# Performance work log

Hardware: AMD Instinct MI355X
Metric: run time of the kernel (lower is better)

## Reference

```python
import jax, jax.numpy as jnp
import numpy as np

EMBED_DIM = 1024
NUM_HEADS = 16
HEAD_DIM = EMBED_DIM // NUM_HEADS
SCALING = HEAD_DIM ** (-0.5)
SEQ = 2048
BSZ = 2


def setup_inputs() -> dict:
    key = jax.random.key(0)
    ks = jax.random.split(key, 11)
    d = {
        "query": jax.random.normal(ks[0], (SEQ, BSZ, EMBED_DIM), dtype=jnp.float32),
        "key": jax.random.normal(ks[1], (SEQ, BSZ, EMBED_DIM), dtype=jnp.float32),
        "value": jax.random.normal(ks[2], (SEQ, BSZ, EMBED_DIM), dtype=jnp.float32),
        "bias_q": jax.random.normal(ks[3], (SEQ, EMBED_DIM), dtype=jnp.float32),
        "bias_k": jax.random.normal(ks[4], (SEQ, EMBED_DIM), dtype=jnp.float32),
        "bias_v": jax.random.normal(ks[5], (SEQ, EMBED_DIM), dtype=jnp.float32),
        # Linear weights (out, in); xavier-ish scale
        "Wq": jax.random.normal(ks[6], (EMBED_DIM, EMBED_DIM), dtype=jnp.float32) * (1.0 / np.sqrt(2 * EMBED_DIM)),
        "Wk": jax.random.normal(ks[7], (EMBED_DIM, EMBED_DIM), dtype=jnp.float32) * (1.0 / np.sqrt(2 * EMBED_DIM)),
        "Wv": jax.random.normal(ks[8], (EMBED_DIM, EMBED_DIM), dtype=jnp.float32) * (1.0 / np.sqrt(2 * EMBED_DIM)),
        "Wo": jax.random.normal(ks[9], (EMBED_DIM, EMBED_DIM), dtype=jnp.float32) * (1.0 / np.sqrt(EMBED_DIM)),
        "bo": jnp.zeros((EMBED_DIM,), dtype=jnp.float32),
    }
    return d


def reference(query, key, value, bias_q, bias_k, bias_v, Wq, Wk, Wv, Wo, bo):
    tgt_len, bsz, embed_dim = query.shape
    # self_attention=True: q, k, v all projected from `query`
    q = (query @ Wq.T + bias_q[:, None, :]) * SCALING   # [T,B,E]
    k = query @ Wk.T + bias_k[:, None, :]                # [T,B,E]
    v = query @ Wv.T + bias_v[:, None, :]                # [T,B,E]

    def split_heads(x):  # [T,B,E] -> [B*H, T, Dh]
        return x.reshape(tgt_len, bsz * NUM_HEADS, HEAD_DIM).transpose(1, 0, 2)

    q, k, v = split_heads(q), split_heads(k), split_heads(v)
    attn_weights = jnp.einsum('btd,bsd->bts', q, k)      # [B*H, T, S]
    attn_weights = jax.nn.softmax(attn_weights, axis=-1)
    attn = jnp.einsum('bts,bsd->btd', attn_weights, v)   # [B*H, T, Dh]
    attn = attn.transpose(1, 0, 2).reshape(tgt_len, bsz, embed_dim)
    attn = attn @ Wo.T + bo
    return (attn, attn_weights)
```

## Files before the change

### kernel.cpp

```cpp
#include <hip/hip_runtime.h>
#include <hip/hip_fp16.h>
#include <cmath>

#define SEQLEN 2048
#define BATCH 2
#define EMB 1024
#define NHEAD 16
#define DHEAD 64
#define NBH 32
#define NROWS 4096

typedef _Float16 f16;
typedef __attribute__((ext_vector_type(4))) _Float16 f16x4;
typedef __attribute__((ext_vector_type(8))) _Float16 f16x8;
typedef __attribute__((ext_vector_type(4))) float f32x4;

__device__ __forceinline__ void gload_lds16(const f16* g, f16* l) {
    __builtin_amdgcn_global_load_lds(
        (const __attribute__((address_space(1))) void*)g,
        (__attribute__((address_space(3))) void*)l, 16, 0, 0);
}

#define QN4 1048576
#define WN4 262144
__global__ __launch_bounds__(256) void cvt_all_kernel(
    const float* __restrict__ query, const float* __restrict__ w0,
    const float* __restrict__ w1, const float* __restrict__ w2,
    const float* __restrict__ w3,
    f16* __restrict__ xh, f16* __restrict__ o0, f16* __restrict__ o1,
    f16* __restrict__ o2, f16* __restrict__ o3)
{
    const int total = QN4 + 4 * WN4;
    for (int i = blockIdx.x * 256 + threadIdx.x; i < total; i += 2048 * 256) {
        const float* src; f16* dst; int off;
        if (i < QN4) { src = query; dst = xh; off = i; }
        else {
            int j = i - QN4;
            int sel = j >> 18;
            off = j & (WN4 - 1);
            switch (sel) {
                case 0: src = w0; dst = o0; break;
                case 1: src = w1; dst = o1; break;
                case 2: src = w2; dst = o2; break;
                default: src = w3; dst = o3; break;
            }
        }
        float4 v = reinterpret_cast<const float4*>(src)[off];
        f16x4 o = {(_Float16)v.x, (_Float16)v.y, (_Float16)v.z, (_Float16)v.w};
        reinterpret_cast<f16x4*>(dst)[off] = o;
    }
}

#define PBK 32

__global__ __launch_bounds__(256, 3) void proj_kernel(
    const f16* __restrict__ xh,
    const f16* __restrict__ Wqh, const f16* __restrict__ Wkh, const f16* __restrict__ Wvh,
    const float* __restrict__ bq, const float* __restrict__ bk, const float* __restrict__ bv,
    f16* __restrict__ qh, f16* __restrict__ kh, f16* __restrict__ vT)
{
    __shared__ __align__(16) f16 smem[16384];

    const int c0f = blockIdx.y * 128;
    const int mode = c0f >> 10;
    const int c0 = c0f & 1023;
    const f16* __restrict__ W = (mode == 0) ? Wqh : (mode == 1 ? Wkh : Wvh);
    const float* __restrict__ bias = (mode == 0) ? bq : (mode == 1 ? bk : bv);
    const int r0 = blockIdx.x * 128;
    const int w = threadIdx.x >> 6;
    const int lane = threadIdx.x & 63;
    const int lr = lane & 15, lg = lane >> 4;
    const int wr = w >> 1, wc = w & 1;

    const int cA0 = w * 64 + lane;
    const int cA1 = 256 + w * 64 + lane;
    const f16* gA0 = xh + (size_t)(r0 + (cA0 >> 2)) * EMB + (cA0 & 3) * 8;
    const f16* gA1 = xh + (size_t)(r0 + (cA1 >> 2)) * EMB + (cA1 & 3) * 8;
    const f16* gB0 = W + (size_t)(c0 + (cA0 >> 2)) * EMB + (cA0 & 3) * 8;
    const f16* gB1 = W + (size_t)(c0 + (cA1 >> 2)) * EMB + (cA1 & 3) * 8;
    const int lds0 = (w * 64) * 8;
    const int lds1 = (256 + w * 64) * 8;

    f32x4 acc[4][4] = {};
    int cur = 0;

    gload_lds16(gA0, smem + lds0);
    gload_lds16(gA1, smem + lds1);
    gload_lds16(gB0, smem + 8192 + lds0);
    gload_lds16(gB1, smem + 8192 + lds1);
    __syncthreads();

    for (int kt = 0; kt < EMB / PBK; ++kt) {
        if (kt + 1 < EMB / PBK) {
            const int ko = (kt + 1) * PBK;
            const int nxt = (cur ^ 1) * 4096;
            gload_lds16(gA0 + ko, smem + nxt + lds0);
            gload_lds16(gA1 + ko, smem + nxt + lds1);
            gload_lds16(gB0 + ko, smem + 8192 + nxt + lds0);
            gload_lds16(gB1 + ko, smem + 8192 + nxt + lds1);
        }
        const f16* Ac = smem + cur * 4096;
        const f16* Bc = smem + 8192 + cur * 4096;
        f16x8 a[4], b[4];
#pragma unroll
        for (int m = 0; m < 4; ++m)
            a[m] = *reinterpret_cast<const f16x8*>(
                &Ac[(wr * 64 + m * 16 + lr) * PBK + lg * 8]);
#pragma unroll
        for (int n = 0; n < 4; ++n)
            b[n] = *reinterpret_cast<const f16x8*>(
                &Bc[(wc * 64 + n * 16 + lr) * PBK + lg * 8]);
#pragma unroll
        for (int m = 0; m < 4; ++m)
#pragma unroll
            for (int n = 0; n < 4; ++n)
                acc[m][n] = __builtin_amdgcn_mfma_f32_16x16x32_f16(b[n], a[m], acc[m][n], 0, 0, 0);
        __syncthreads();
        cur ^= 1;
    }

    if (mode != 2) {
        f16* __restrict__ dst = (mode == 0) ? qh : kh;
        const float sc = (mode == 0) ? 0.125f : 1.0f;
#pragma unroll
        for (int m = 0; m < 4; ++m) {
            const int row = r0 + wr * 64 + m * 16 + lr;
            const int t = row >> 1, bb = row & 1;
#pragma unroll
            for (int n = 0; n < 4; ++n) {
                const int col0 = c0 + wc * 64 + n * 16 + lg * 4;
                float4 b4 = *reinterpret_cast<const float4*>(&bias[(size_t)t * EMB + col0]);
                f16x4 pk = {(_Float16)((acc[m][n][0] + b4.x) * sc),
                            (_Float16)((acc[m][n][1] + b4.y) * sc),
                            (_Float16)((acc[m][n][2] + b4.z) * sc),
                            (_Float16)((acc[m][n][3] + b4.w) * sc)};
                const int h = col0 >> 6, d0 = col0 & 63;
                const int bhi = bb * NHEAD + h;
                *reinterpret_cast<f16x4*>(
                    &dst[((size_t)bhi * SEQLEN + t) * DHEAD + d0]) = pk;
            }
        }
    } else {
        f16* T = smem;
#pragma unroll
        for (int p = 0; p < 2; ++p) {
            if (wr == p) {
#pragma unroll
                for (int m = 0; m < 4; ++m) {
                    const int row = r0 + p * 64 + m * 16 + lr;
                    const int t = row >> 1;
#pragma unroll
                    for (int n = 0; n < 4; ++n) {
                        const int ci0 = wc * 64 + n * 16 + lg * 4;
                        float4 b4 = *reinterpret_cast<const float4*>(
                            &bias[(size_t)t * EMB + c0 + ci0]);
                        f16x4 pk = {(_Float16)(acc[m][n][0] + b4.x),
                                    (_Float16)(acc[m][n][1] + b4.y),
                                    (_Float16)(acc[m][n][2] + b4.z),
                                    (_Float16)(acc[m][n][3] + b4.w)};
                        *reinterpret_cast<f16x4*>(&T[(m * 16 + lr) * 132 + ci0]) = pk;
                    }
                }
            }
            __syncthreads();
            {
                const int dd = threadIdx.x & 63;
                const int hh = (threadIdx.x >> 6) & 1;
                const int bb2 = threadIdx.x >> 7;
                const int bhi2 = bb2 * NHEAD + ((c0 + hh * 64) >> 6);
                const int tbase = (r0 + p * 64) >> 1;
                f16* __restrict__ vrow =
                    vT + ((size_t)bhi2 * 64 + (tbase >> 5)) * (DHEAD * 32) + dd * 32;
#pragma unroll
                for (int j8 = 0; j8 < 4; ++j8) {
                    f16x8 pk8;
#pragma unroll
                    for (int jj = 0; jj < 8; ++jj)
                        pk8[jj] = T[(bb2 + 2 * (j8 * 8 + jj)) * 132 + hh * 64 + dd];
                    *reinterpret_cast<f16x8*>(&vrow[j8 * 8]) = pk8;
                }
            }
            __syncthreads();
        }
    }
}

#define QBLK 32
#define SCHUNK 128
#define TP 136
#define RP 2080

__global__ __launch_bounds__(1024, 1) void attn_kernel(
    const f16* __restrict__ qh, const f16* __restrict__ kh, const f16* __restrict__ vT,
    float* __restrict__ Pout, f16* __restrict__ ctx)
{
    __shared__ __align__(16) f16 tbuf[16][QBLK * TP];
    __shared__ float lsum[QBLK][16];
    __shared__ float inv_l[QBLK];
    float* red = (float*)&tbuf[0][0];

    const int id = blockIdx.x;
    const int idx = id >> 3;
    const int bh = ((id & 7) << 2) + (idx >> 6);
    const int t0 = (idx & 63) * QBLK;

    const int w = threadIdx.x >> 6;
    const int lane = threadIdx.x & 63;
    const int lr = lane & 15, lg = lane >> 4;
    const int sbase = w * SCHUNK;

    const f16* __restrict__ qb = qh + (size_t)bh * SEQLEN * DHEAD;
    const f16* __restrict__ kb = kh + (size_t)bh * SEQLEN * DHEAD;
    const f16* __restrict__ vb = vT + (size_t)bh * DHEAD * SEQLEN;

    f16x8 qf[2][2];
#pragma unroll
    for (int tt = 0; tt < 2; ++tt)
#pragma unroll
        for (int kc = 0; kc < 2; ++kc)
            qf[tt][kc] = *reinterpret_cast<const f16x8*>(
                qb + (size_t)(t0 + tt * 16 + lr) * DHEAD + kc * 32 + lg * 8);

    f16x4 ev[2][8];
    float rowsum[2] = {0.f, 0.f};
#pragma unroll
    for (int st = 0; st < 8; ++st) {
        const f16* krow = kb + (size_t)(sbase + st * 16 + lr) * DHEAD;
        f16x8 kf0 = *reinterpret_cast<const f16x8*>(krow + lg * 8);
        f16x8 kf1 = *reinterpret_cast<const f16x8*>(krow + 32 + lg * 8);
#pragma unroll
        for (int tt = 0; tt < 2; ++tt) {
            f32x4 sa = {};
            sa = __builtin_amdgcn_mfma_f32_16x16x32_f16(kf0, qf[tt][0], sa, 0, 0, 0);
            sa = __builtin_amdgcn_mfma_f32_16x16x32_f16(kf1, qf[tt][1], sa, 0, 0, 0);
            float ps = 0.f;
#pragma unroll
            for (int e = 0; e < 4; ++e) {
                float Ev = __expf(sa[e]) * 0.0625f;
                ev[tt][st][e] = (_Float16)Ev;
                ps += Ev;
            }
            rowsum[tt] += ps;
        }
    }

#pragma unroll
    for (int tt = 0; tt < 2; ++tt) {
        float v = rowsum[tt];
        v += __shfl_xor(v, 16);
        v += __shfl_xor(v, 32);
        if (lg == 0) lsum[tt * 16 + lr][w] = v;
    }

    f16* mybuf = &tbuf[w][0];
#pragma unroll
    for (int tt = 0; tt < 2; ++tt)
#pragma unroll
        for (int st = 0; st < 8; ++st)
            *reinterpret_cast<f16x4*>(
                &mybuf[(tt * 16 + lr) * TP + st * 16 + lg * 4]) = ev[tt][st];

    __syncthreads();
    if (threadIdx.x < QBLK) {
        float s = 0.f;
#pragma unroll
        for (int i = 0; i < 16; ++i) s += lsum[threadIdx.x][i];
        inv_l[threadIdx.x] = 1.0f / s;
    }
    __syncthreads();

    float* __restrict__ Pt =
        Pout + (size_t)bh * SEQLEN * SEQLEN + (size_t)t0 * SEQLEN;
#pragma unroll
    for (int j = 0; j < 2; ++j) {
        const int t = w * 2 + j;
        const float inv = inv_l[t];
#pragma unroll
        for (int cc = 0; cc < 8; ++cc) {
            const int chunk = cc * 2 + (lane >> 5);
            const int col = (lane & 31) * 4;
            f16x4 e4 = *reinterpret_cast<const f16x4*>(
                &tbuf[chunk][t * TP + col]);
            f32x4 o = {(float)e4[0] * inv, (float)e4[1] * inv,
                       (float)e4[2] * inv, (float)e4[3] * inv};
            __builtin_nontemporal_store(o,
                reinterpret_cast<f32x4*>(&Pt[(size_t)t * SEQLEN + cc * 256 + lane * 4]));
        }
    }

    f32x4 accO[2][4] = {};
#pragma unroll
    for (int c = 0; c < 4; ++c) {
        f16x8 pa0 = *reinterpret_cast<const f16x8*>(&mybuf[lr * TP + c * 32 + lg * 8]);
        f16x8 pa1 = *reinterpret_cast<const f16x8*>(&mybuf[(16 + lr) * TP + c * 32 + lg * 8]);
        const f16* vchunk = vb + (size_t)(w * 4 + c) * (DHEAD * 32);
#pragma unroll
        for (int dt = 0; dt < 4; ++dt) {
            f16x8 vf = *reinterpret_cast<const f16x8*>(
                vchunk + (dt * 16 + lr) * 32 + lg * 8);
            accO[0][dt] = __builtin_amdgcn_mfma_f32_16x16x32_f16(pa0, vf, accO[0][dt], 0, 0, 0);
            accO[1][dt] = __builtin_amdgcn_mfma_f32_16x16x32_f16(pa1, vf, accO[1][dt], 0, 0, 0);
        }
    }
    __syncthreads();

#pragma unroll
    for (int tt = 0; tt < 2; ++tt)
#pragma unroll
        for (int dt = 0; dt < 4; ++dt)
#pragma unroll
            for (int e = 0; e < 4; ++e)
                red[(size_t)w * RP + (tt * 16 + lg * 4 + e) * 65 + dt * 16 + lr] =
                    accO[tt][dt][e];
    __syncthreads();

    const int b = bh >> 4, h = bh & 15;
    for (int o = threadIdx.x; o < QBLK * DHEAD; o += 1024) {
        const int t = o >> 6, d = o & 63;
        float s = 0.f;
#pragma unroll
        for (int i = 0; i < 16; ++i) s += red[(size_t)i * RP + t * 65 + d];
        s *= inv_l[t];
        ctx[(size_t)((t0 + t) * BATCH + b) * EMB + h * DHEAD + d] = (f16)s;
    }
}

__global__ __launch_bounds__(256, 4) void oproj_kernel(
    const f16* __restrict__ ctx, const f16* __restrict__ Woh,
    const float* __restrict__ bo, float* __restrict__ out)
{
    __shared__ __align__(16) f16 smem[12288];
    const int r0 = blockIdx.x * 64;
    const int c0 = blockIdx.y * 128;
    const int w = threadIdx.x >> 6;
    const int lane = threadIdx.x & 63;
    const int lr = lane & 15, lg = lane >> 4;
    const int wr = w >> 1, wc = w & 1;

    const int cA = threadIdx.x;
    const f16* gA = ctx + (size_t)(r0 + (cA >> 2)) * EMB + (cA & 3) * 8;
    const f16* gB0 = Woh + (size_t)(c0 + (cA >> 2)) * EMB + (cA & 3) * 8;
    const f16* gB1 = Woh + (size_t)(c0 + 64 + (cA >> 2)) * EMB + (cA & 3) * 8;
    const int ldsA = (w * 64) * 8;
    const int ldsB0 = (w * 64) * 8;
    const int ldsB1 = (256 + w * 64) * 8;

    f32x4 acc[2][4] = {};
    int cur = 0;

    gload_lds16(gA, smem + ldsA);
    gload_lds16(gB0, smem + 4096 + ldsB0);
    gload_lds16(gB1, smem + 4096 + ldsB1);
    __syncthreads();

    for (int kt = 0; kt < EMB / PBK; ++kt) {
        if (kt + 1 < EMB / PBK) {
            const int ko = (kt + 1) * PBK;
            const int nxtA = (cur ^ 1) * 2048;
            const int nxtB = 4096 + (cur ^ 1) * 4096;
            gload_lds16(gA + ko, smem + nxtA + ldsA);
            gload_lds16(gB0 + ko, smem + nxtB + ldsB0);
            gload_lds16(gB1 + ko, smem + nxtB + ldsB1);
        }
        const f16* Ac = smem + cur * 2048;
        const f16* Bc = smem + 4096 + cur * 4096;
        f16x8 a[2], b[4];
#pragma unroll
        for (int m = 0; m < 2; ++m)
            a[m] = *reinterpret_cast<const f16x8*>(
                &Ac[(wr * 32 + m * 16 + lr) * PBK + lg * 8]);
#pragma unroll
        for (int n = 0; n < 4; ++n)
            b[n] = *reinterpret_cast<const f16x8*>(
                &Bc[(wc * 64 + n * 16 + lr) * PBK + lg * 8]);
#pragma unroll
        for (int m = 0; m < 2; ++m)
#pragma unroll
            for (int n = 0; n < 4; ++n)
                acc[m][n] = __builtin_amdgcn_mfma_f32_16x16x32_f16(b[n], a[m], acc[m][n], 0, 0, 0);
        __syncthreads();
        cur ^= 1;
    }

#pragma unroll
    for (int m = 0; m < 2; ++m) {
        const int row = r0 + wr * 32 + m * 16 + lr;
#pragma unroll
        for (int n = 0; n < 4; ++n) {
            const int col0 = c0 + wc * 64 + n * 16 + lg * 4;
            float4 b4 = *reinterpret_cast<const float4*>(&bo[col0]);
            f32x4 o = {acc[m][n][0] + b4.x, acc[m][n][1] + b4.y,
                       acc[m][n][2] + b4.z, acc[m][n][3] + b4.w};
            __builtin_nontemporal_store(o,
                reinterpret_cast<f32x4*>(&out[(size_t)row * EMB + col0]));
        }
    }
}

extern "C" void kernel_launch(void* const* d_in, const int* in_sizes, int n_in,
                              void* d_out, int out_size, void* d_ws, size_t ws_size,
                              hipStream_t stream) {
    const float* query = (const float*)d_in[0];
    const float* bq = (const float*)d_in[3];
    const float* bk = (const float*)d_in[4];
    const float* bv = (const float*)d_in[5];
    const float* Wq = (const float*)d_in[6];
    const float* Wk = (const float*)d_in[7];
    const float* Wv = (const float*)d_in[8];
    const float* Wo = (const float*)d_in[9];
    const float* bo = (const float*)d_in[10];

    char* ws = (char*)d_ws;
    f16* xh  = (f16*)(ws);
    f16* Wqh = (f16*)(ws + ( 8u << 20));
    f16* Wkh = (f16*)(ws + (10u << 20));
    f16* Wvh = (f16*)(ws + (12u << 20));
    f16* Woh = (f16*)(ws + (14u << 20));
    f16* qhp = (f16*)(ws + (16u << 20));
    f16* khp = (f16*)(ws + (24u << 20));
    f16* vTp = (f16*)(ws + (32u << 20));
    f16* ctx = (f16*)(ws + (40u << 20));

    float* outA = (float*)d_out;
    float* outP = (float*)d_out + (size_t)SEQLEN * BATCH * EMB;

    cvt_all_kernel<<<2048, 256, 0, stream>>>(query, Wq, Wk, Wv, Wo,
                                             xh, Wqh, Wkh, Wvh, Woh);

    proj_kernel<<<dim3(NROWS / 128, 3072 / 128), 256, 0, stream>>>(
        xh, Wqh, Wkh, Wvh, bq, bk, bv, qhp, khp, vTp);

    attn_kernel<<<SEQLEN / QBLK * NBH, 1024, 0, stream>>>(qhp, khp, vTp, outP, ctx);

    oproj_kernel<<<dim3(NROWS / 64, EMB / 128), 256, 0, stream>>>(ctx, Woh, bo, outA);
}
```

Measured before the change: 228.1 us.

## Double query block per attention CTA and overlap P stores with PV MFMAs

Each attention block now processes 64 query rows instead of 32, halving the grid and the number of times each K/V chunk is read per head. Because LDS only holds eight wave chunks at once, the waves are split into two halves. One half writes the normalized probability matrix to global memory while the other half runs the P·V MFMAs, then the roles swap after the second half of the exp values is staged. The cross-wave reduction of the output is done in two passes to fit the LDS budget. In exchange, each wave keeps twice as many registers live (ev and accO), and the extra barriers may hurt occupancy and scheduling.

```diff
diff --git a/kernel.cpp b/kernel.cpp
--- a/kernel.cpp
+++ b/kernel.cpp
@@ -185,24 +185,25 @@
     }
 }
 
-#define QBLK 32
+#define QBLK 64
 #define SCHUNK 128
 #define TP 136
+#define CHSZ (QBLK * TP)
 #define RP 2080
 
 __global__ __launch_bounds__(1024, 1) void attn_kernel(
     const f16* __restrict__ qh, const f16* __restrict__ kh, const f16* __restrict__ vT,
     float* __restrict__ Pout, f16* __restrict__ ctx)
 {
-    __shared__ __align__(16) f16 tbuf[16][QBLK * TP];
+    __shared__ __align__(16) f16 tbuf[8 * CHSZ];
     __shared__ float lsum[QBLK][16];
     __shared__ float inv_l[QBLK];
-    float* red = (float*)&tbuf[0][0];
+    float* red = (float*)&tbuf[0];
 
     const int id = blockIdx.x;
     const int idx = id >> 3;
-    const int bh = ((id & 7) << 2) + (idx >> 6);
-    const int t0 = (idx & 63) * QBLK;
+    const int bh = ((id & 7) << 2) + (idx >> 5);
+    const int t0 = (idx & 31) * QBLK;
 
     const int w = threadIdx.x >> 6;
     const int lane = threadIdx.x & 63;
@@ -213,23 +214,23 @@
     const f16* __restrict__ kb = kh + (size_t)bh * SEQLEN * DHEAD;
     const f16* __restrict__ vb = vT + (size_t)bh * DHEAD * SEQLEN;
 
-    f16x8 qf[2][2];
-#pragma unroll
-    for (int tt = 0; tt < 2; ++tt)
+    f16x8 qf[4][2];
+#pragma unroll
+    for (int tt = 0; tt < 4; ++tt)
 #pragma unroll
         for (int kc = 0; kc < 2; ++kc)
             qf[tt][kc] = *reinterpret_cast<const f16x8*>(
                 qb + (size_t)(t0 + tt * 16 + lr) * DHEAD + kc * 32 + lg * 8);
 
-    f16x4 ev[2][8];
-    float rowsum[2] = {0.f, 0.f};
+    f16x4 ev[4][8];
+    float rowsum[4] = {0.f, 0.f, 0.f, 0.f};
 #pragma unroll
     for (int st = 0; st < 8; ++st) {
         const f16* krow = kb + (size_t)(sbase + st * 16 + lr) * DHEAD;
         f16x8 kf0 = *reinterpret_cast<const f16x8*>(krow + lg * 8);
         f16x8 kf1 = *reinterpret_cast<const f16x8*>(krow + 32 + lg * 8);
 #pragma unroll
-        for (int tt = 0; tt < 2; ++tt) {
+        for (int tt = 0; tt < 4; ++tt) {
             f32x4 sa = {};
             sa = __builtin_amdgcn_mfma_f32_16x16x32_f16(kf0, qf[tt][0], sa, 0, 0, 0);
             sa = __builtin_amdgcn_mfma_f32_16x16x32_f16(kf1, qf[tt][1], sa, 0, 0, 0);
@@ -245,21 +246,22 @@
     }
 
 #pragma unroll
-    for (int tt = 0; tt < 2; ++tt) {
+    for (int tt = 0; tt < 4; ++tt) {
         float v = rowsum[tt];
         v += __shfl_xor(v, 16);
         v += __shfl_xor(v, 32);
         if (lg == 0) lsum[tt * 16 + lr][w] = v;
     }
 
-    f16* mybuf = &tbuf[w][0];
-#pragma unroll
-    for (int tt = 0; tt < 2; ++tt)
-#pragma unroll
-        for (int st = 0; st < 8; ++st)
-            *reinterpret_cast<f16x4*>(
-                &mybuf[(tt * 16 + lr) * TP + st * 16 + lg * 4]) = ev[tt][st];
-
+    if (w < 8) {
+        f16* mybuf = &tbuf[w * CHSZ];
+#pragma unroll
+        for (int tt = 0; tt < 4; ++tt)
+#pragma unroll
+            for (int st = 0; st < 8; ++st)
+                *reinterpret_cast<f16x4*>(
+                    &mybuf[(tt * 16 + lr) * TP + st * 16 + lg * 4]) = ev[tt][st];
+    }
     __syncthreads();
     if (threadIdx.x < QBLK) {
         float s = 0.f;
@@ -271,57 +273,126 @@
 
     float* __restrict__ Pt =
         Pout + (size_t)bh * SEQLEN * SEQLEN + (size_t)t0 * SEQLEN;
-#pragma unroll
-    for (int j = 0; j < 2; ++j) {
-        const int t = w * 2 + j;
-        const float inv = inv_l[t];
-#pragma unroll
-        for (int cc = 0; cc < 8; ++cc) {
-            const int chunk = cc * 2 + (lane >> 5);
-            const int col = (lane & 31) * 4;
-            f16x4 e4 = *reinterpret_cast<const f16x4*>(
-                &tbuf[chunk][t * TP + col]);
-            f32x4 o = {(float)e4[0] * inv, (float)e4[1] * inv,
-                       (float)e4[2] * inv, (float)e4[3] * inv};
-            __builtin_nontemporal_store(o,
-                reinterpret_cast<f32x4*>(&Pt[(size_t)t * SEQLEN + cc * 256 + lane * 4]));
-        }
-    }
-
-    f32x4 accO[2][4] = {};
-#pragma unroll
-    for (int c = 0; c < 4; ++c) {
-        f16x8 pa0 = *reinterpret_cast<const f16x8*>(&mybuf[lr * TP + c * 32 + lg * 8]);
-        f16x8 pa1 = *reinterpret_cast<const f16x8*>(&mybuf[(16 + lr) * TP + c * 32 + lg * 8]);
-        const f16* vchunk = vb + (size_t)(w * 4 + c) * (DHEAD * 32);
-#pragma unroll
-        for (int dt = 0; dt < 4; ++dt) {
-            f16x8 vf = *reinterpret_cast<const f16x8*>(
-                vchunk + (dt * 16 + lr) * 32 + lg * 8);
-            accO[0][dt] = __builtin_amdgcn_mfma_f32_16x16x32_f16(pa0, vf, accO[0][dt], 0, 0, 0);
-            accO[1][dt] = __builtin_amdgcn_mfma_f32_16x16x32_f16(pa1, vf, accO[1][dt], 0, 0, 0);
-        }
-    }
-    __syncthreads();
-
-#pragma unroll
-    for (int tt = 0; tt < 2; ++tt)
-#pragma unroll
-        for (int dt = 0; dt < 4; ++dt)
-#pragma unroll
-            for (int e = 0; e < 4; ++e)
-                red[(size_t)w * RP + (tt * 16 + lg * 4 + e) * 65 + dt * 16 + lr] =
-                    accO[tt][dt][e];
+    f32x4 accO[4][4] = {};
+
+    if (w >= 8) {
+        const int r0w = (w - 8) * 8;
+#pragma unroll
+        for (int r = 0; r < 8; ++r) {
+            const int t = r0w + r;
+            const float inv = inv_l[t];
+#pragma unroll
+            for (int i = 0; i < 4; ++i) {
+                const int chunk = i * 2 + (lane >> 5);
+                const int col = (lane & 31) * 4;
+                f16x4 e4 = *reinterpret_cast<const f16x4*>(
+                    &tbuf[chunk * CHSZ + t * TP + col]);
+                f32x4 o = {(float)e4[0] * inv, (float)e4[1] * inv,
+                           (float)e4[2] * inv, (float)e4[3] * inv};
+                __builtin_nontemporal_store(o,
+                    reinterpret_cast<f32x4*>(&Pt[(size_t)t * SEQLEN + i * 256 + lane * 4]));
+            }
+        }
+    } else {
+        const f16* mybuf = &tbuf[w * CHSZ];
+#pragma unroll
+        for (int c = 0; c < 4; ++c) {
+            const f16* vchunk = vb + (size_t)(w * 4 + c) * (DHEAD * 32);
+            f16x8 vf[4];
+#pragma unroll
+            for (int dt = 0; dt < 4; ++dt)
+                vf[dt] = *reinterpret_cast<const f16x8*>(
+                    vchunk + (dt * 16 + lr) * 32 + lg * 8);
+#pragma unroll
+            for (int tt = 0; tt < 4; ++tt) {
+                f16x8 pa = *reinterpret_cast<const f16x8*>(
+                    &mybuf[(tt * 16 + lr) * TP + c * 32 + lg * 8]);
+#pragma unroll
+                for (int dt = 0; dt < 4; ++dt)
+                    accO[tt][dt] = __builtin_amdgcn_mfma_f32_16x16x32_f16(
+                        pa, vf[dt], accO[tt][dt], 0, 0, 0);
+            }
+        }
+    }
+    __syncthreads();
+
+    if (w >= 8) {
+        f16* mybuf = &tbuf[(w - 8) * CHSZ];
+#pragma unroll
+        for (int tt = 0; tt < 4; ++tt)
+#pragma unroll
+            for (int st = 0; st < 8; ++st)
+                *reinterpret_cast<f16x4*>(
+                    &mybuf[(tt * 16 + lr) * TP + st * 16 + lg * 4]) = ev[tt][st];
+    }
+    __syncthreads();
+
+    if (w < 8) {
+        const int r0w = w * 8;
+#pragma unroll
+        for (int r = 0; r < 8; ++r) {
+            const int t = r0w + r;
+            const float inv = inv_l[t];
+#pragma unroll
+            for (int i = 0; i < 4; ++i) {
+                const int chunk = i * 2 + (lane >> 5);
+                const int col = (lane & 31) * 4;
+                f16x4 e4 = *reinterpret_cast<const f16x4*>(
+                    &tbuf[chunk * CHSZ + t * TP + col]);
+                f32x4 o = {(float)e4[0] * inv, (float)e4[1] * inv,
+                           (float)e4[2] * inv, (float)e4[3] * inv};
+                __builtin_nontemporal_store(o,
+                    reinterpret_cast<f32x4*>(
+                        &Pt[(size_t)t * SEQLEN + 1024 + i * 256 + lane * 4]));
+            }
+        }
+    } else {
+        const f16* mybuf = &tbuf[(w - 8) * CHSZ];
+#pragma unroll
+        for (int c = 0; c < 4; ++c) {
+            const f16* vchunk = vb + (size_t)(w * 4 + c) * (DHEAD * 32);
+            f16x8 vf[4];
+#pragma unroll
+            for (int dt = 0; dt < 4; ++dt)
+                vf[dt] = *reinterpret_cast<const f16x8*>(
+                    vchunk + (dt * 16 + lr) * 32 + lg * 8);
+#pragma unroll
+            for (int tt = 0; tt < 4; ++tt) {
+                f16x8 pa = *reinterpret_cast<const f16x8*>(
+                    &mybuf[(tt * 16 + lr) * TP + c * 32 + lg * 8]);
+#pragma unroll
+                for (int dt = 0; dt < 4; ++dt)
+                    accO[tt][dt] = __builtin_amdgcn_mfma_f32_16x16x32_f16(
+                        pa, vf[dt], accO[tt][dt], 0, 0, 0);
+            }
+        }
+    }
     __syncthreads();
 
     const int b = bh >> 4, h = bh & 15;
-    for (int o = threadIdx.x; o < QBLK * DHEAD; o += 1024) {
-        const int t = o >> 6, d = o & 63;
-        float s = 0.f;
-#pragma unroll
-        for (int i = 0; i < 16; ++i) s += red[(size_t)i * RP + t * 65 + d];
-        s *= inv_l[t];
-        ctx[(size_t)((t0 + t) * BATCH + b) * EMB + h * DHEAD + d] = (f16)s;
+#pragma unroll
+    for (int half = 0; half < 2; ++half) {
+#pragma unroll
+        for (int tl = 0; tl < 2; ++tl) {
+            const int tt = half * 2 + tl;
+#pragma unroll
+            for (int dt = 0; dt < 4; ++dt)
+#pragma unroll
+                for (int e = 0; e < 4; ++e)
+                    red[(size_t)w * RP + (tl * 16 + lg * 4 + e) * 65 + dt * 16 + lr] =
+                        accO[tt][dt][e];
+        }
+        __syncthreads();
+        for (int o = threadIdx.x; o < 32 * DHEAD; o += 1024) {
+            const int t = o >> 6, d = o & 63;
+            float s = 0.f;
+#pragma unroll
+            for (int i = 0; i < 16; ++i) s += red[(size_t)i * RP + t * 65 + d];
+            const int tg = half * 32 + t;
+            s *= inv_l[tg];
+            ctx[(size_t)((t0 + tg) * BATCH + b) * EMB + h * DHEAD + d] = (f16)s;
+        }
+        __syncthreads();
     }
 }
 
```

Result: slower. 293.5 us (+28.7%).
